# Kernel optimization log

Hardware: AMD Instinct MI355X
Metric: run time of the kernel (lower is better)

Reference implementation:

```python
import jax, jax.numpy as jnp
import numpy as np

IN_CH = 256
BOT = IN_CH // 2  # bottleneck channels
B, W, H = 4, 64, 64


def setup_inputs() -> dict:
    key = jax.random.key(0)
    ks = jax.random.split(key, 10)
    s_in = 1.0 / np.sqrt(IN_CH)   # torch Conv2d default init scale (kaiming-ish bound)
    s_bt = 1.0 / np.sqrt(BOT)
    return {
        "X": jax.random.normal(ks[0], (B, IN_CH, W, H), dtype=jnp.float32),
        "Wq": jax.random.uniform(ks[1], (BOT, IN_CH), jnp.float32, -s_in, s_in),
        "bq": jax.random.uniform(ks[2], (BOT,), jnp.float32, -s_in, s_in),
        "Wk": jax.random.uniform(ks[3], (BOT, IN_CH), jnp.float32, -s_in, s_in),
        "bk": jax.random.uniform(ks[4], (BOT,), jnp.float32, -s_in, s_in),
        "Wv": jax.random.uniform(ks[5], (BOT, IN_CH), jnp.float32, -s_in, s_in),
        "bv": jax.random.uniform(ks[6], (BOT,), jnp.float32, -s_in, s_in),
        "Wo": jax.random.uniform(ks[7], (IN_CH, BOT), jnp.float32, -s_bt, s_bt),
        "bo": jax.random.uniform(ks[8], (IN_CH,), jnp.float32, -s_bt, s_bt),
        "gamma": 0.1 * jax.random.normal(ks[9], (1,), dtype=jnp.float32),
    }


def reference(X, Wq, bq, Wk, bk, Wv, bv, Wo, bo, gamma):
    b, c, w, h = X.shape
    n = w * h
    Xf = X.reshape(b, c, n)  # [b, c, n] — 1x1 conv == per-pixel linear
    q = jnp.einsum('oc,bcn->bon', Wq, Xf) + bq[None, :, None]  # [b, c/2, n]
    k = jnp.einsum('oc,bcn->bon', Wk, Xf) + bk[None, :, None]
    v = jnp.einsum('oc,bcn->bon', Wv, Xf) + bv[None, :, None]
    # score[b,i,j] = sum_c q[b,c,i] * k[b,c,j]; softmax over dim=1 (query index i)
    score = jnp.einsum('bci,bcj->bij', q, k)          # [b, n, n]
    attn = jax.nn.softmax(score, axis=1)
    out = jnp.einsum('bci,bij->bcj', v, attn)         # [b, c/2, n]
    out = jnp.einsum('oc,bcn->bon', Wo, out) + bo[None, :, None]  # [b, c, n]
    out = out.reshape(b, c, w, h)
    return gamma[0] * out + X
```

## Files before the change

### kernel.cpp

```cpp
#include <hip/hip_runtime.h>
#include <math.h>

#define NBATCH 4
#define CIN    256
#define CBOT   128
#define NPIX   4096
#define NPART  4
#define LOG2E  1.44269504f

typedef __attribute__((ext_vector_type(4))) float f32x4;
typedef __attribute__((ext_vector_type(8))) short bf16x8;

__device__ __forceinline__ unsigned short f2bf(float f) {
    union { float f; unsigned u; } v; v.f = f;
    unsigned r = (v.u + 0x7FFFu + ((v.u >> 16) & 1u)) >> 16;
    return (unsigned short)r;
}

__global__ __launch_bounds__(256) void k_wcvt(
    const float* __restrict__ Wq, const float* __restrict__ Wk,
    const float* __restrict__ Wv, const float* __restrict__ Wo,
    unsigned short* __restrict__ Wb)
{
    const int f4 = (blockIdx.x * 256 + threadIdx.x) * 4;
    const int reg = f4 >> 15, loc = f4 & 32767;
    const float* __restrict__ W = (reg == 0) ? Wq : (reg == 1) ? Wk : (reg == 2) ? Wv : Wo;
    const float sc = (reg == 1) ? LOG2E : 1.f;
    float4 v = *(const float4*)(W + loc);
    ushort4 u;
    u.x = f2bf(v.x * sc); u.y = f2bf(v.y * sc);
    u.z = f2bf(v.z * sc); u.w = f2bf(v.w * sc);
    *(ushort4*)&Wb[f4] = u;
}

__global__ __launch_bounds__(256) void k_xt(
    const float* __restrict__ X, unsigned short* __restrict__ Xt)
{
    __shared__ float T[64][65];
    const int tid = threadIdx.x;
    const int pbase = blockIdx.x * 64;
    const int c0    = blockIdx.y * 64;
    const int b     = blockIdx.z;
#pragma unroll
    for (int k = 0; k < 4; ++k) {
        int f = tid + 256 * k;
        int cl = f >> 4, p4 = (f & 15) << 2;
        float4 v = *(const float4*)(X + (size_t)b * CIN * NPIX + (size_t)(c0 + cl) * NPIX + pbase + p4);
        T[cl][p4 + 0] = v.x; T[cl][p4 + 1] = v.y;
        T[cl][p4 + 2] = v.z; T[cl][p4 + 3] = v.w;
    }
    __syncthreads();
#pragma unroll
    for (int k = 0; k < 4; ++k) {
        int f = tid + 256 * k;
        int p = f >> 4, c4 = (f & 15) << 2;
        ushort4 u;
        u.x = f2bf(T[c4 + 0][p]); u.y = f2bf(T[c4 + 1][p]);
        u.z = f2bf(T[c4 + 2][p]); u.w = f2bf(T[c4 + 3][p]);
        *(ushort4*)&Xt[((size_t)b * NPIX + pbase + p) * CIN + c0 + c4] = u;
    }
}

__global__ __launch_bounds__(256) void k_qkv(
    const unsigned short* __restrict__ Xt,
    const unsigned short* __restrict__ Wb,
    const float* __restrict__ bq, const float* __restrict__ bk,
    const float* __restrict__ bv,
    unsigned short* __restrict__ Qt, unsigned short* __restrict__ Kt,
    unsigned short* __restrict__ Vt)
{
    const int tid = threadIdx.x;
    const int wv = tid >> 6, lane = tid & 63;
    const int grp = lane & 15, quad = lane >> 4;
    const int pbase = blockIdx.x * 32;
    const int b     = blockIdx.y;
    const unsigned short* __restrict__ Xb  = Xt + (size_t)b * NPIX * CIN;
    const unsigned short* __restrict__ Wqb = Wb;
    const unsigned short* __restrict__ Wkb = Wb + 32768;
    const unsigned short* __restrict__ Wvb = Wb + 65536;
    const int obase = 32 * wv;

    f32x4 aQ[2][2], aK[2][2], aV[2][2];
#pragma unroll
    for (int mt = 0; mt < 2; ++mt)
#pragma unroll
        for (int nt = 0; nt < 2; ++nt) {
            aQ[mt][nt] = (f32x4)0.f; aK[mt][nt] = (f32x4)0.f; aV[mt][nt] = (f32x4)0.f;
        }

    for (int ks = 0; ks < 8; ++ks) {
        bf16x8 bx[2];
#pragma unroll
        for (int nt = 0; nt < 2; ++nt)
            bx[nt] = *(const bf16x8*)&Xb[(size_t)(pbase + nt * 16 + grp) * CIN + ks * 32 + quad * 8];
        bf16x8 wq_[2], wk_[2], wv_[2];
#pragma unroll
        for (int mt = 0; mt < 2; ++mt) {
            const size_t roff = (size_t)(obase + mt * 16 + grp) * CIN + ks * 32 + quad * 8;
            wq_[mt] = *(const bf16x8*)&Wqb[roff];
            wk_[mt] = *(const bf16x8*)&Wkb[roff];
            wv_[mt] = *(const bf16x8*)&Wvb[roff];
        }
#pragma unroll
        for (int mt = 0; mt < 2; ++mt)
#pragma unroll
            for (int nt = 0; nt < 2; ++nt) {
                aQ[mt][nt] = __builtin_amdgcn_mfma_f32_16x16x32_bf16(wq_[mt], bx[nt], aQ[mt][nt], 0, 0, 0);
                aK[mt][nt] = __builtin_amdgcn_mfma_f32_16x16x32_bf16(wk_[mt], bx[nt], aK[mt][nt], 0, 0, 0);
                aV[mt][nt] = __builtin_amdgcn_mfma_f32_16x16x32_bf16(bx[mt], wv_[nt], aV[mt][nt], 0, 0, 0);
            }
    }

    unsigned short* Qb_ = Qt + (size_t)b * NPIX * CBOT;
    unsigned short* Kb_ = Kt + (size_t)b * NPIX * CBOT;
#pragma unroll
    for (int mt = 0; mt < 2; ++mt) {
        int o0 = obase + mt * 16 + quad * 4;
        float b4q[4], b4k[4];
#pragma unroll
        for (int r = 0; r < 4; ++r) { b4q[r] = bq[o0 + r]; b4k[r] = bk[o0 + r] * LOG2E; }
#pragma unroll
        for (int nt = 0; nt < 2; ++nt) {
            int p = pbase + nt * 16 + grp;
            ushort4 uq, uk;
            uq.x = f2bf(aQ[mt][nt][0] + b4q[0]); uq.y = f2bf(aQ[mt][nt][1] + b4q[1]);
            uq.z = f2bf(aQ[mt][nt][2] + b4q[2]); uq.w = f2bf(aQ[mt][nt][3] + b4q[3]);
            uk.x = f2bf(aK[mt][nt][0] + b4k[0]); uk.y = f2bf(aK[mt][nt][1] + b4k[1]);
            uk.z = f2bf(aK[mt][nt][2] + b4k[2]); uk.w = f2bf(aK[mt][nt][3] + b4k[3]);
            *(ushort4*)&Qb_[(size_t)p * CBOT + o0] = uq;
            *(ushort4*)&Kb_[(size_t)p * CBOT + o0] = uk;
        }
    }
    unsigned short* Vb_ = Vt + (size_t)b * CBOT * NPIX;
#pragma unroll
    for (int nt = 0; nt < 2; ++nt) {
        int o = obase + nt * 16 + grp;
        float bb = bv[o];
#pragma unroll
        for (int mt = 0; mt < 2; ++mt) {
            int p0 = pbase + mt * 16 + quad * 4;
            ushort4 u;
            u.x = f2bf(aV[mt][nt][0] + bb); u.y = f2bf(aV[mt][nt][1] + bb);
            u.z = f2bf(aV[mt][nt][2] + bb); u.w = f2bf(aV[mt][nt][3] + bb);
            *(ushort4*)&Vb_[(size_t)o * NPIX + p0] = u;
        }
    }
}

__global__ __launch_bounds__(256, 2) void k_flash(
    const unsigned short* __restrict__ Qt,
    const unsigned short* __restrict__ Kt,
    const unsigned short* __restrict__ Vt,
    unsigned short* __restrict__ Opart,
    float* __restrict__ Lpart)
{
    __shared__ __align__(16) unsigned short Qs[64][136];
    __shared__ __align__(16) unsigned short Vs[128][72];
    __shared__ __align__(16) unsigned short Ps[128][72];
    const int tid  = threadIdx.x;
    const int wv   = tid >> 6, lane = tid & 63;
    const int grp  = lane & 15, quad = lane >> 4;
    const int jblk = blockIdx.x * 128;
    const int part = blockIdx.y;
    const int b    = blockIdx.z;
    const int tbeg = part * (64 / NPART);
    const int tend = tbeg + (64 / NPART);
    const unsigned short* __restrict__ Qb = Qt + (size_t)b * NPIX * CBOT;
    const unsigned short* __restrict__ Kb = Kt + (size_t)b * NPIX * CBOT;
    const unsigned short* __restrict__ Vb = Vt + (size_t)b * CBOT * NPIX;

    bf16x8 aq[2][4];
#pragma unroll
    for (int set = 0; set < 2; ++set)
#pragma unroll
        for (int ks = 0; ks < 4; ++ks)
            aq[set][ks] = *(const bf16x8*)&Kb[
                (size_t)(jblk + wv * 32 + set * 16 + grp) * CBOT + ks * 32 + quad * 8];

    bf16x8 bones;
#pragma unroll
    for (int t = 0; t < 8; ++t) bones[t] = (short)0x3F80;

    f32x4 o[2][8];
#pragma unroll
    for (int set = 0; set < 2; ++set)
#pragma unroll
        for (int ct = 0; ct < 8; ++ct) o[set][ct] = (f32x4)0.f;
    f32x4 lacc[2] = {(f32x4)0.f, (f32x4)0.f};

    const int qrow = tid >> 4, qch = tid & 15;
    const int vrow = tid >> 3, vch = tid & 7;
    bf16x8 qreg[4], vreg[4];
#pragma unroll
    for (int k = 0; k < 4; ++k) {
        qreg[k] = *(const bf16x8*)&Qb[(size_t)(tbeg * 64 + qrow + 16 * k) * CBOT + qch * 8];
        vreg[k] = *(const bf16x8*)&Vb[(size_t)(vrow + 32 * k) * NPIX + tbeg * 64 + vch * 8];
    }

    for (int it = tbeg; it < tend; ++it) {
        __syncthreads();
#pragma unroll
        for (int k = 0; k < 4; ++k) {
            *(bf16x8*)&Qs[qrow + 16 * k][qch * 8] = qreg[k];
            *(bf16x8*)&Vs[vrow + 32 * k][vch * 8] = vreg[k];
        }
        __syncthreads();
        if (it + 1 < tend) {
            const int i1 = (it + 1) * 64;
#pragma unroll
            for (int k = 0; k < 4; ++k) {
                qreg[k] = *(const bf16x8*)&Qb[(size_t)(i1 + qrow + 16 * k) * CBOT + qch * 8];
                vreg[k] = *(const bf16x8*)&Vb[(size_t)(vrow + 32 * k) * NPIX + i1 + vch * 8];
            }
        }

        f32x4 sf[2][4];
#pragma unroll
        for (int set = 0; set < 2; ++set)
#pragma unroll
            for (int nt = 0; nt < 4; ++nt) sf[set][nt] = (f32x4)0.f;
#pragma unroll
        for (int nt = 0; nt < 4; ++nt)
#pragma unroll
            for (int ks = 0; ks < 4; ++ks) {
                bf16x8 bq_ = *(const bf16x8*)&Qs[nt * 16 + grp][ks * 32 + quad * 8];
                sf[0][nt] = __builtin_amdgcn_mfma_f32_16x16x32_bf16(aq[0][ks], bq_, sf[0][nt], 0, 0, 0);
                sf[1][nt] = __builtin_amdgcn_mfma_f32_16x16x32_bf16(aq[1][ks], bq_, sf[1][nt], 0, 0, 0);
            }

#pragma unroll
        for (int set = 0; set < 2; ++set)
#pragma unroll
            for (int nt = 0; nt < 4; ++nt)
#pragma unroll
                for (int r = 0; r < 4; ++r)
                    Ps[wv * 32 + set * 16 + quad * 4 + r][nt * 16 + grp] =
                        f2bf(exp2f(sf[set][nt][r]));

        bf16x8 af[2][2];
#pragma unroll
        for (int set = 0; set < 2; ++set)
#pragma unroll
            for (int ks2 = 0; ks2 < 2; ++ks2)
                af[set][ks2] = *(const bf16x8*)&Ps[wv * 32 + set * 16 + grp][ks2 * 32 + quad * 8];

#pragma unroll
        for (int ct = 0; ct < 8; ++ct)
#pragma unroll
            for (int ks2 = 0; ks2 < 2; ++ks2) {
                bf16x8 bv_ = *(const bf16x8*)&Vs[ct * 16 + grp][ks2 * 32 + quad * 8];
                o[0][ct] = __builtin_amdgcn_mfma_f32_16x16x32_bf16(af[0][ks2], bv_, o[0][ct], 0, 0, 0);
                o[1][ct] = __builtin_amdgcn_mfma_f32_16x16x32_bf16(af[1][ks2], bv_, o[1][ct], 0, 0, 0);
            }
#pragma unroll
        for (int set = 0; set < 2; ++set) {
            lacc[set] = __builtin_amdgcn_mfma_f32_16x16x32_bf16(af[set][0], bones, lacc[set], 0, 0, 0);
            lacc[set] = __builtin_amdgcn_mfma_f32_16x16x32_bf16(af[set][1], bones, lacc[set], 0, 0, 0);
        }
    }

    unsigned short* Ob = Opart + ((size_t)(part * NBATCH + b) * NPIX + jblk) * CBOT;
#pragma unroll
    for (int set = 0; set < 2; ++set)
#pragma unroll
        for (int ct = 0; ct < 8; ++ct)
#pragma unroll
            for (int r = 0; r < 4; ++r)
                Ob[(size_t)(wv * 32 + set * 16 + quad * 4 + r) * CBOT + ct * 16 + grp] =
                    f2bf(o[set][ct][r]);
    if (grp == 0) {
#pragma unroll
        for (int set = 0; set < 2; ++set)
#pragma unroll
            for (int r = 0; r < 4; ++r)
                Lpart[(size_t)(part * NBATCH + b) * NPIX + jblk + wv * 32 + set * 16 + quad * 4 + r] =
                    lacc[set][r];
    }
}

__global__ __launch_bounds__(256) void k_oproj(
    const unsigned short* __restrict__ Opart, const float* __restrict__ Lpart,
    const unsigned short* __restrict__ Wob, const float* __restrict__ bo,
    const float* __restrict__ gamma, const float* __restrict__ X,
    float* __restrict__ Out)
{
    const int tid = threadIdx.x;
    const int wv = tid >> 6, lane = tid & 63;
    const int grp = lane & 15, quad = lane >> 4;
    const int pbase = blockIdx.x * 32;
    const int b     = blockIdx.y;
    const int obase = 64 * wv;

    f32x4 acc[2][4];
#pragma unroll
    for (int mt = 0; mt < 2; ++mt)
#pragma unroll
        for (int nt = 0; nt < 4; ++nt) acc[mt][nt] = (f32x4)0.f;

    for (int ks = 0; ks < 4; ++ks) {
        bf16x8 bw[4];
#pragma unroll
        for (int nt = 0; nt < 4; ++nt)
            bw[nt] = *(const bf16x8*)&Wob[(size_t)(obase + nt * 16 + grp) * CBOT + ks * 32 + quad * 8];
#pragma unroll
        for (int mt = 0; mt < 2; ++mt) {
            int p = pbase + mt * 16 + grp;
#pragma unroll
            for (int part = 0; part < NPART; ++part) {
                bf16x8 ao = *(const bf16x8*)&Opart[
                    ((size_t)(part * NBATCH + b) * NPIX + p) * CBOT + ks * 32 + quad * 8];
#pragma unroll
                for (int nt = 0; nt < 4; ++nt)
                    acc[mt][nt] = __builtin_amdgcn_mfma_f32_16x16x32_bf16(ao, bw[nt], acc[mt][nt], 0, 0, 0);
            }
        }
    }

    float linv[2][4];
#pragma unroll
    for (int mt = 0; mt < 2; ++mt)
#pragma unroll
        for (int r = 0; r < 4; ++r) {
            int p = pbase + mt * 16 + quad * 4 + r;
            float ls = 0.f;
#pragma unroll
            for (int part = 0; part < NPART; ++part)
                ls += Lpart[(size_t)(part * NBATCH + b) * NPIX + p];
            linv[mt][r] = 1.f / ls;
        }
    float g = gamma[0];
#pragma unroll
    for (int nt = 0; nt < 4; ++nt) {
        int o = obase + nt * 16 + grp;
        float bb = bo[o];
#pragma unroll
        for (int mt = 0; mt < 2; ++mt) {
            int p0 = pbase + mt * 16 + quad * 4;
            size_t base = (size_t)b * CIN * NPIX + (size_t)o * NPIX + p0;
            float4 x4 = *(const float4*)(X + base);
            float4 r4;
            r4.x = g * (acc[mt][nt][0] * linv[mt][0] + bb) + x4.x;
            r4.y = g * (acc[mt][nt][1] * linv[mt][1] + bb) + x4.y;
            r4.z = g * (acc[mt][nt][2] * linv[mt][2] + bb) + x4.z;
            r4.w = g * (acc[mt][nt][3] * linv[mt][3] + bb) + x4.w;
            *(float4*)(Out + base) = r4;
        }
    }
}

extern "C" void kernel_launch(void* const* d_in, const int* in_sizes, int n_in,
                              void* d_out, int out_size, void* d_ws, size_t ws_size,
                              hipStream_t stream)
{
    (void)in_sizes; (void)n_in; (void)out_size; (void)ws_size;
    const float* X     = (const float*)d_in[0];
    const float* Wq    = (const float*)d_in[1];
    const float* bq    = (const float*)d_in[2];
    const float* Wk    = (const float*)d_in[3];
    const float* bk    = (const float*)d_in[4];
    const float* Wv    = (const float*)d_in[5];
    const float* bv    = (const float*)d_in[6];
    const float* Wo    = (const float*)d_in[7];
    const float* bo    = (const float*)d_in[8];
    const float* gamma = (const float*)d_in[9];
    float* out = (float*)d_out;

    const size_t BNC = (size_t)NBATCH * NPIX * CBOT;
    unsigned short* Qt    = (unsigned short*)d_ws;
    unsigned short* Kt    = Qt + BNC;
    unsigned short* Vt    = Kt + BNC;
    unsigned short* Opart = Vt + BNC;
    unsigned short* Xt    = Opart;
    float*          Lpart = (float*)(Opart + (size_t)NPART * BNC);
    unsigned short* Wb    = (unsigned short*)(Lpart + (size_t)NPART * NBATCH * NPIX);

    k_wcvt <<<dim3(128),               256, 0, stream>>>(Wq, Wk, Wv, Wo, Wb);
    k_xt   <<<dim3(64, 4, NBATCH),     256, 0, stream>>>(X, Xt);
    k_qkv  <<<dim3(128, NBATCH),       256, 0, stream>>>(Xt, Wb, bq, bk, bv, Qt, Kt, Vt);
    k_flash<<<dim3(32, NPART, NBATCH), 256, 0, stream>>>(Qt, Kt, Vt, Opart, Lpart);
    k_oproj<<<dim3(128, NBATCH),       256, 0, stream>>>(Opart, Lpart, Wb + 98304, bo, gamma, X, out);
}
```

Measured before the change: 174.5 us.

## Fuse QKV, flash, and output projection into persistent kernel with grid barriers

Merges weight conversion into the X transpose kernel. The QKV projection, flash attention and output projection kernels become one 512-block kernel separated by software grid barriers built on atomics. The aim is to remove launch overhead and inter-kernel gaps across five launches. It relies on all 512 blocks being co-resident (launch bounds of 2 blocks per CU, 256 CUs). The barrier has a spin timeout that could silently break correctness, and it adds atomic spin cost.

```diff
diff --git a/kernel.cpp b/kernel.cpp
--- a/kernel.cpp
+++ b/kernel.cpp
@@ -6,6 +6,7 @@
 #define CBOT   128
 #define NPIX   4096
 #define NPART  4
+#define NBLK   512
 #define LOG2E  1.44269504f
 
 typedef __attribute__((ext_vector_type(4))) float f32x4;
@@ -17,27 +18,52 @@
     return (unsigned short)r;
 }
 
-__global__ __launch_bounds__(256) void k_wcvt(
+__device__ __forceinline__ void gridbar(unsigned* cnt, unsigned* gen) {
+    __syncthreads();
+    if (threadIdx.x == 0) {
+        unsigned g = __hip_atomic_load(gen, __ATOMIC_RELAXED, __HIP_MEMORY_SCOPE_AGENT);
+        unsigned a = __hip_atomic_fetch_add(cnt, 1u, __ATOMIC_ACQ_REL, __HIP_MEMORY_SCOPE_AGENT);
+        if (a == NBLK - 1u) {
+            __hip_atomic_store(cnt, 0u, __ATOMIC_RELAXED, __HIP_MEMORY_SCOPE_AGENT);
+            __hip_atomic_store(gen, g + 1u, __ATOMIC_RELEASE, __HIP_MEMORY_SCOPE_AGENT);
+        } else {
+            int spins = 0;
+            while (__hip_atomic_load(gen, __ATOMIC_ACQUIRE, __HIP_MEMORY_SCOPE_AGENT) == g) {
+                __builtin_amdgcn_s_sleep(2);
+                if (++spins > (1 << 22)) break;
+            }
+        }
+    }
+    __syncthreads();
+}
+
+__global__ __launch_bounds__(256) void k_prep(
+    const float* __restrict__ X,
     const float* __restrict__ Wq, const float* __restrict__ Wk,
     const float* __restrict__ Wv, const float* __restrict__ Wo,
-    unsigned short* __restrict__ Wb)
-{
-    const int f4 = (blockIdx.x * 256 + threadIdx.x) * 4;
-    const int reg = f4 >> 15, loc = f4 & 32767;
-    const float* __restrict__ W = (reg == 0) ? Wq : (reg == 1) ? Wk : (reg == 2) ? Wv : Wo;
-    const float sc = (reg == 1) ? LOG2E : 1.f;
-    float4 v = *(const float4*)(W + loc);
-    ushort4 u;
-    u.x = f2bf(v.x * sc); u.y = f2bf(v.y * sc);
-    u.z = f2bf(v.z * sc); u.w = f2bf(v.w * sc);
-    *(ushort4*)&Wb[f4] = u;
-}
-
-__global__ __launch_bounds__(256) void k_xt(
-    const float* __restrict__ X, unsigned short* __restrict__ Xt)
+    unsigned short* __restrict__ Xt, unsigned short* __restrict__ Wb,
+    unsigned* __restrict__ Bar)
 {
     __shared__ float T[64][65];
     const int tid = threadIdx.x;
+    if (blockIdx.y == 4) {
+        const int gid = blockIdx.z * 64 + blockIdx.x;
+        if (gid < 128) {
+            const int f4 = (gid * 256 + tid) * 4;
+            const int reg = f4 >> 15, loc = f4 & 32767;
+            const float* __restrict__ W = (reg == 0) ? Wq : (reg == 1) ? Wk
+                                        : (reg == 2) ? Wv : Wo;
+            const float sc = (reg == 1) ? LOG2E : 1.f;
+            float4 v = *(const float4*)(W + loc);
+            ushort4 u;
+            u.x = f2bf(v.x * sc); u.y = f2bf(v.y * sc);
+            u.z = f2bf(v.z * sc); u.w = f2bf(v.w * sc);
+            *(ushort4*)&Wb[f4] = u;
+        } else if (gid == 128 && tid < 8) {
+            Bar[tid] = 0u;
+        }
+        return;
+    }
     const int pbase = blockIdx.x * 64;
     const int c0    = blockIdx.y * 64;
     const int b     = blockIdx.z;
@@ -61,289 +87,286 @@
     }
 }
 
-__global__ __launch_bounds__(256) void k_qkv(
-    const unsigned short* __restrict__ Xt,
+__global__ __launch_bounds__(256, 2) void k_mega(
+    const unsigned short* Xt,
     const unsigned short* __restrict__ Wb,
     const float* __restrict__ bq, const float* __restrict__ bk,
     const float* __restrict__ bv,
     unsigned short* __restrict__ Qt, unsigned short* __restrict__ Kt,
-    unsigned short* __restrict__ Vt)
-{
-    const int tid = threadIdx.x;
-    const int wv = tid >> 6, lane = tid & 63;
-    const int grp = lane & 15, quad = lane >> 4;
-    const int pbase = blockIdx.x * 32;
-    const int b     = blockIdx.y;
-    const unsigned short* __restrict__ Xb  = Xt + (size_t)b * NPIX * CIN;
-    const unsigned short* __restrict__ Wqb = Wb;
-    const unsigned short* __restrict__ Wkb = Wb + 32768;
-    const unsigned short* __restrict__ Wvb = Wb + 65536;
-    const int obase = 32 * wv;
-
-    f32x4 aQ[2][2], aK[2][2], aV[2][2];
-#pragma unroll
-    for (int mt = 0; mt < 2; ++mt)
-#pragma unroll
-        for (int nt = 0; nt < 2; ++nt) {
-            aQ[mt][nt] = (f32x4)0.f; aK[mt][nt] = (f32x4)0.f; aV[mt][nt] = (f32x4)0.f;
-        }
-
-    for (int ks = 0; ks < 8; ++ks) {
-        bf16x8 bx[2];
-#pragma unroll
-        for (int nt = 0; nt < 2; ++nt)
-            bx[nt] = *(const bf16x8*)&Xb[(size_t)(pbase + nt * 16 + grp) * CIN + ks * 32 + quad * 8];
-        bf16x8 wq_[2], wk_[2], wv_[2];
-#pragma unroll
-        for (int mt = 0; mt < 2; ++mt) {
-            const size_t roff = (size_t)(obase + mt * 16 + grp) * CIN + ks * 32 + quad * 8;
-            wq_[mt] = *(const bf16x8*)&Wqb[roff];
-            wk_[mt] = *(const bf16x8*)&Wkb[roff];
-            wv_[mt] = *(const bf16x8*)&Wvb[roff];
-        }
-#pragma unroll
-        for (int mt = 0; mt < 2; ++mt)
-#pragma unroll
-            for (int nt = 0; nt < 2; ++nt) {
-                aQ[mt][nt] = __builtin_amdgcn_mfma_f32_16x16x32_bf16(wq_[mt], bx[nt], aQ[mt][nt], 0, 0, 0);
-                aK[mt][nt] = __builtin_amdgcn_mfma_f32_16x16x32_bf16(wk_[mt], bx[nt], aK[mt][nt], 0, 0, 0);
-                aV[mt][nt] = __builtin_amdgcn_mfma_f32_16x16x32_bf16(bx[mt], wv_[nt], aV[mt][nt], 0, 0, 0);
-            }
-    }
-
-    unsigned short* Qb_ = Qt + (size_t)b * NPIX * CBOT;
-    unsigned short* Kb_ = Kt + (size_t)b * NPIX * CBOT;
-#pragma unroll
-    for (int mt = 0; mt < 2; ++mt) {
-        int o0 = obase + mt * 16 + quad * 4;
-        float b4q[4], b4k[4];
-#pragma unroll
-        for (int r = 0; r < 4; ++r) { b4q[r] = bq[o0 + r]; b4k[r] = bk[o0 + r] * LOG2E; }
-#pragma unroll
-        for (int nt = 0; nt < 2; ++nt) {
-            int p = pbase + nt * 16 + grp;
-            ushort4 uq, uk;
-            uq.x = f2bf(aQ[mt][nt][0] + b4q[0]); uq.y = f2bf(aQ[mt][nt][1] + b4q[1]);
-            uq.z = f2bf(aQ[mt][nt][2] + b4q[2]); uq.w = f2bf(aQ[mt][nt][3] + b4q[3]);
-            uk.x = f2bf(aK[mt][nt][0] + b4k[0]); uk.y = f2bf(aK[mt][nt][1] + b4k[1]);
-            uk.z = f2bf(aK[mt][nt][2] + b4k[2]); uk.w = f2bf(aK[mt][nt][3] + b4k[3]);
-            *(ushort4*)&Qb_[(size_t)p * CBOT + o0] = uq;
-            *(ushort4*)&Kb_[(size_t)p * CBOT + o0] = uk;
-        }
-    }
-    unsigned short* Vb_ = Vt + (size_t)b * CBOT * NPIX;
-#pragma unroll
-    for (int nt = 0; nt < 2; ++nt) {
-        int o = obase + nt * 16 + grp;
-        float bb = bv[o];
-#pragma unroll
-        for (int mt = 0; mt < 2; ++mt) {
-            int p0 = pbase + mt * 16 + quad * 4;
-            ushort4 u;
-            u.x = f2bf(aV[mt][nt][0] + bb); u.y = f2bf(aV[mt][nt][1] + bb);
-            u.z = f2bf(aV[mt][nt][2] + bb); u.w = f2bf(aV[mt][nt][3] + bb);
-            *(ushort4*)&Vb_[(size_t)o * NPIX + p0] = u;
-        }
-    }
-}
-
-__global__ __launch_bounds__(256, 2) void k_flash(
-    const unsigned short* __restrict__ Qt,
-    const unsigned short* __restrict__ Kt,
-    const unsigned short* __restrict__ Vt,
-    unsigned short* __restrict__ Opart,
-    float* __restrict__ Lpart)
+    unsigned short* __restrict__ Vt,
+    unsigned short* Opart, float* __restrict__ Lpart,
+    const float* __restrict__ bo, const float* __restrict__ gamma,
+    const float* __restrict__ X, float* __restrict__ Out,
+    unsigned* Bar)
 {
     __shared__ __align__(16) unsigned short Qs[64][136];
     __shared__ __align__(16) unsigned short Vs[128][72];
     __shared__ __align__(16) unsigned short Ps[128][72];
+
     const int tid  = threadIdx.x;
+    const int bid  = blockIdx.x;
     const int wv   = tid >> 6, lane = tid & 63;
     const int grp  = lane & 15, quad = lane >> 4;
-    const int jblk = blockIdx.x * 128;
-    const int part = blockIdx.y;
-    const int b    = blockIdx.z;
-    const int tbeg = part * (64 / NPART);
-    const int tend = tbeg + (64 / NPART);
-    const unsigned short* __restrict__ Qb = Qt + (size_t)b * NPIX * CBOT;
-    const unsigned short* __restrict__ Kb = Kt + (size_t)b * NPIX * CBOT;
-    const unsigned short* __restrict__ Vb = Vt + (size_t)b * CBOT * NPIX;
-
-    bf16x8 aq[2][4];
-#pragma unroll
-    for (int set = 0; set < 2; ++set)
-#pragma unroll
-        for (int ks = 0; ks < 4; ++ks)
-            aq[set][ks] = *(const bf16x8*)&Kb[
-                (size_t)(jblk + wv * 32 + set * 16 + grp) * CBOT + ks * 32 + quad * 8];
-
-    bf16x8 bones;
-#pragma unroll
-    for (int t = 0; t < 8; ++t) bones[t] = (short)0x3F80;
-
-    f32x4 o[2][8];
-#pragma unroll
-    for (int set = 0; set < 2; ++set)
-#pragma unroll
-        for (int ct = 0; ct < 8; ++ct) o[set][ct] = (f32x4)0.f;
-    f32x4 lacc[2] = {(f32x4)0.f, (f32x4)0.f};
-
-    const int qrow = tid >> 4, qch = tid & 15;
-    const int vrow = tid >> 3, vch = tid & 7;
-    bf16x8 qreg[4], vreg[4];
-#pragma unroll
-    for (int k = 0; k < 4; ++k) {
-        qreg[k] = *(const bf16x8*)&Qb[(size_t)(tbeg * 64 + qrow + 16 * k) * CBOT + qch * 8];
-        vreg[k] = *(const bf16x8*)&Vb[(size_t)(vrow + 32 * k) * NPIX + tbeg * 64 + vch * 8];
-    }
-
-    for (int it = tbeg; it < tend; ++it) {
-        __syncthreads();
+
+    {
+        const int pbase = (bid & 127) * 32;
+        const int b     = bid >> 7;
+        const unsigned short* Xb  = Xt + (size_t)b * NPIX * CIN;
+        const unsigned short* __restrict__ Wqb = Wb;
+        const unsigned short* __restrict__ Wkb = Wb + 32768;
+        const unsigned short* __restrict__ Wvb = Wb + 65536;
+        const int obase = 32 * wv;
+
+        f32x4 aQ[2][2], aK[2][2], aV[2][2];
+#pragma unroll
+        for (int mt = 0; mt < 2; ++mt)
+#pragma unroll
+            for (int nt = 0; nt < 2; ++nt) {
+                aQ[mt][nt] = (f32x4)0.f; aK[mt][nt] = (f32x4)0.f; aV[mt][nt] = (f32x4)0.f;
+            }
+
+        for (int ks = 0; ks < 8; ++ks) {
+            bf16x8 bx[2];
+#pragma unroll
+            for (int nt = 0; nt < 2; ++nt)
+                bx[nt] = *(const bf16x8*)&Xb[(size_t)(pbase + nt * 16 + grp) * CIN + ks * 32 + quad * 8];
+            bf16x8 wq_[2], wk_[2], wv_[2];
+#pragma unroll
+            for (int mt = 0; mt < 2; ++mt) {
+                const size_t roff = (size_t)(obase + mt * 16 + grp) * CIN + ks * 32 + quad * 8;
+                wq_[mt] = *(const bf16x8*)&Wqb[roff];
+                wk_[mt] = *(const bf16x8*)&Wkb[roff];
+                wv_[mt] = *(const bf16x8*)&Wvb[roff];
+            }
+#pragma unroll
+            for (int mt = 0; mt < 2; ++mt)
+#pragma unroll
+                for (int nt = 0; nt < 2; ++nt) {
+                    aQ[mt][nt] = __builtin_amdgcn_mfma_f32_16x16x32_bf16(wq_[mt], bx[nt], aQ[mt][nt], 0, 0, 0);
+                    aK[mt][nt] = __builtin_amdgcn_mfma_f32_16x16x32_bf16(wk_[mt], bx[nt], aK[mt][nt], 0, 0, 0);
+                    aV[mt][nt] = __builtin_amdgcn_mfma_f32_16x16x32_bf16(bx[mt], wv_[nt], aV[mt][nt], 0, 0, 0);
+                }
+        }
+
+        unsigned short* Qb_ = Qt + (size_t)b * NPIX * CBOT;
+        unsigned short* Kb_ = Kt + (size_t)b * NPIX * CBOT;
+#pragma unroll
+        for (int mt = 0; mt < 2; ++mt) {
+            int o0 = obase + mt * 16 + quad * 4;
+            float b4q[4], b4k[4];
+#pragma unroll
+            for (int r = 0; r < 4; ++r) { b4q[r] = bq[o0 + r]; b4k[r] = bk[o0 + r] * LOG2E; }
+#pragma unroll
+            for (int nt = 0; nt < 2; ++nt) {
+                int p = pbase + nt * 16 + grp;
+                ushort4 uq, uk;
+                uq.x = f2bf(aQ[mt][nt][0] + b4q[0]); uq.y = f2bf(aQ[mt][nt][1] + b4q[1]);
+                uq.z = f2bf(aQ[mt][nt][2] + b4q[2]); uq.w = f2bf(aQ[mt][nt][3] + b4q[3]);
+                uk.x = f2bf(aK[mt][nt][0] + b4k[0]); uk.y = f2bf(aK[mt][nt][1] + b4k[1]);
+                uk.z = f2bf(aK[mt][nt][2] + b4k[2]); uk.w = f2bf(aK[mt][nt][3] + b4k[3]);
+                *(ushort4*)&Qb_[(size_t)p * CBOT + o0] = uq;
+                *(ushort4*)&Kb_[(size_t)p * CBOT + o0] = uk;
+            }
+        }
+        unsigned short* Vb_ = Vt + (size_t)b * CBOT * NPIX;
+#pragma unroll
+        for (int nt = 0; nt < 2; ++nt) {
+            int o = obase + nt * 16 + grp;
+            float bb = bv[o];
+#pragma unroll
+            for (int mt = 0; mt < 2; ++mt) {
+                int p0 = pbase + mt * 16 + quad * 4;
+                ushort4 u;
+                u.x = f2bf(aV[mt][nt][0] + bb); u.y = f2bf(aV[mt][nt][1] + bb);
+                u.z = f2bf(aV[mt][nt][2] + bb); u.w = f2bf(aV[mt][nt][3] + bb);
+                *(ushort4*)&Vb_[(size_t)o * NPIX + p0] = u;
+            }
+        }
+    }
+
+    gridbar(Bar, Bar + 1);
+
+    {
+        const int jblk = (bid & 31) * 128;
+        const int part = (bid >> 5) & 3;
+        const int b    = bid >> 7;
+        const int tbeg = part * (64 / NPART);
+        const int tend = tbeg + (64 / NPART);
+        const unsigned short* __restrict__ Qb = Qt + (size_t)b * NPIX * CBOT;
+        const unsigned short* __restrict__ Kb = Kt + (size_t)b * NPIX * CBOT;
+        const unsigned short* __restrict__ Vb = Vt + (size_t)b * CBOT * NPIX;
+
+        bf16x8 aq[2][4];
+#pragma unroll
+        for (int set = 0; set < 2; ++set)
+#pragma unroll
+            for (int ks = 0; ks < 4; ++ks)
+                aq[set][ks] = *(const bf16x8*)&Kb[
+                    (size_t)(jblk + wv * 32 + set * 16 + grp) * CBOT + ks * 32 + quad * 8];
+
+        bf16x8 bones;
+#pragma unroll
+        for (int t = 0; t < 8; ++t) bones[t] = (short)0x3F80;
+
+        f32x4 o[2][8];
+#pragma unroll
+        for (int set = 0; set < 2; ++set)
+#pragma unroll
+            for (int ct = 0; ct < 8; ++ct) o[set][ct] = (f32x4)0.f;
+        f32x4 lacc[2] = {(f32x4)0.f, (f32x4)0.f};
+
+        const int qrow = tid >> 4, qch = tid & 15;
+        const int vrow = tid >> 3, vch = tid & 7;
+        bf16x8 qreg[4], vreg[4];
 #pragma unroll
         for (int k = 0; k < 4; ++k) {
-            *(bf16x8*)&Qs[qrow + 16 * k][qch * 8] = qreg[k];
-            *(bf16x8*)&Vs[vrow + 32 * k][vch * 8] = vreg[k];
-        }
-        __syncthreads();
-        if (it + 1 < tend) {
-            const int i1 = (it + 1) * 64;
+            qreg[k] = *(const bf16x8*)&Qb[(size_t)(tbeg * 64 + qrow + 16 * k) * CBOT + qch * 8];
+            vreg[k] = *(const bf16x8*)&Vb[(size_t)(vrow + 32 * k) * NPIX + tbeg * 64 + vch * 8];
+        }
+
+        for (int it = tbeg; it < tend; ++it) {
+            __syncthreads();
 #pragma unroll
             for (int k = 0; k < 4; ++k) {
-                qreg[k] = *(const bf16x8*)&Qb[(size_t)(i1 + qrow + 16 * k) * CBOT + qch * 8];
-                vreg[k] = *(const bf16x8*)&Vb[(size_t)(vrow + 32 * k) * NPIX + i1 + vch * 8];
-            }
-        }
-
-        f32x4 sf[2][4];
+                *(bf16x8*)&Qs[qrow + 16 * k][qch * 8] = qreg[k];
+                *(bf16x8*)&Vs[vrow + 32 * k][vch * 8] = vreg[k];
+            }
+            __syncthreads();
+            if (it + 1 < tend) {
+                const int i1 = (it + 1) * 64;
+#pragma unroll
+                for (int k = 0; k < 4; ++k) {
+                    qreg[k] = *(const bf16x8*)&Qb[(size_t)(i1 + qrow + 16 * k) * CBOT + qch * 8];
+                    vreg[k] = *(const bf16x8*)&Vb[(size_t)(vrow + 32 * k) * NPIX + i1 + vch * 8];
+                }
+            }
+
+            f32x4 sf[2][4];
+#pragma unroll
+            for (int set = 0; set < 2; ++set)
+#pragma unroll
+                for (int nt = 0; nt < 4; ++nt) sf[set][nt] = (f32x4)0.f;
+#pragma unroll
+            for (int nt = 0; nt < 4; ++nt)
+#pragma unroll
+                for (int ks = 0; ks < 4; ++ks) {
+                    bf16x8 bq_ = *(const bf16x8*)&Qs[nt * 16 + grp][ks * 32 + quad * 8];
+                    sf[0][nt] = __builtin_amdgcn_mfma_f32_16x16x32_bf16(aq[0][ks], bq_, sf[0][nt], 0, 0, 0);
+                    sf[1][nt] = __builtin_amdgcn_mfma_f32_16x16x32_bf16(aq[1][ks], bq_, sf[1][nt], 0, 0, 0);
+                }
+
+#pragma unroll
+            for (int set = 0; set < 2; ++set)
+#pragma unroll
+                for (int nt = 0; nt < 4; ++nt)
+#pragma unroll
+                    for (int r = 0; r < 4; ++r)
+                        Ps[wv * 32 + set * 16 + quad * 4 + r][nt * 16 + grp] =
+                            f2bf(exp2f(sf[set][nt][r]));
+
+            bf16x8 af[2][2];
+#pragma unroll
+            for (int set = 0; set < 2; ++set)
+#pragma unroll
+                for (int ks2 = 0; ks2 < 2; ++ks2)
+                    af[set][ks2] = *(const bf16x8*)&Ps[wv * 32 + set * 16 + grp][ks2 * 32 + quad * 8];
+
+#pragma unroll
+            for (int ct = 0; ct < 8; ++ct)
+#pragma unroll
+                for (int ks2 = 0; ks2 < 2; ++ks2) {
+                    bf16x8 bv_ = *(const bf16x8*)&Vs[ct * 16 + grp][ks2 * 32 + quad * 8];
+                    o[0][ct] = __builtin_amdgcn_mfma_f32_16x16x32_bf16(af[0][ks2], bv_, o[0][ct], 0, 0, 0);
+                    o[1][ct] = __builtin_amdgcn_mfma_f32_16x16x32_bf16(af[1][ks2], bv_, o[1][ct], 0, 0, 0);
+                }
+#pragma unroll
+            for (int set = 0; set < 2; ++set) {
+                lacc[set] = __builtin_amdgcn_mfma_f32_16x16x32_bf16(af[set][0], bones, lacc[set], 0, 0, 0);
+                lacc[set] = __builtin_amdgcn_mfma_f32_16x16x32_bf16(af[set][1], bones, lacc[set], 0, 0, 0);
+            }
+        }
+
+        unsigned short* Ob = Opart + ((size_t)(part * NBATCH + b) * NPIX + jblk) * CBOT;
 #pragma unroll
         for (int set = 0; set < 2; ++set)
 #pragma unroll
-            for (int nt = 0; nt < 4; ++nt) sf[set][nt] = (f32x4)0.f;
-#pragma unroll
-        for (int nt = 0; nt < 4; ++nt)
-#pragma unroll
-            for (int ks = 0; ks < 4; ++ks) {
-                bf16x8 bq_ = *(const bf16x8*)&Qs[nt * 16 + grp][ks * 32 + quad * 8];
-                sf[0][nt] = __builtin_amdgcn_mfma_f32_16x16x32_bf16(aq[0][ks], bq_, sf[0][nt], 0, 0, 0);
-                sf[1][nt] = __builtin_amdgcn_mfma_f32_16x16x32_bf16(aq[1][ks], bq_, sf[1][nt], 0, 0, 0);
-            }
-
-#pragma unroll
-        for (int set = 0; set < 2; ++set)
+            for (int ct = 0; ct < 8; ++ct)
+#pragma unroll
+                for (int r = 0; r < 4; ++r)
+                    Ob[(size_t)(wv * 32 + set * 16 + quad * 4 + r) * CBOT + ct * 16 + grp] =
+                        f2bf(o[set][ct][r]);
+        if (grp == 0) {
+#pragma unroll
+            for (int set = 0; set < 2; ++set)
+#pragma unroll
+                for (int r = 0; r < 4; ++r)
+                    Lpart[(size_t)(part * NBATCH + b) * NPIX + jblk + wv * 32 + set * 16 + quad * 4 + r] =
+                        lacc[set][r];
+        }
+    }
+
+    gridbar(Bar, Bar + 1);
+
+    {
+        const int pbase = (bid & 127) * 32;
+        const int b     = bid >> 7;
+        const unsigned short* __restrict__ Wob = Wb + 98304;
+        const int obase = 64 * wv;
+
+        f32x4 acc[2][4];
+#pragma unroll
+        for (int mt = 0; mt < 2; ++mt)
+#pragma unroll
+            for (int nt = 0; nt < 4; ++nt) acc[mt][nt] = (f32x4)0.f;
+
+        for (int ks = 0; ks < 4; ++ks) {
+            bf16x8 bw[4];
 #pragma unroll
             for (int nt = 0; nt < 4; ++nt)
-#pragma unroll
-                for (int r = 0; r < 4; ++r)
-                    Ps[wv * 32 + set * 16 + quad * 4 + r][nt * 16 + grp] =
-                        f2bf(exp2f(sf[set][nt][r]));
-
-        bf16x8 af[2][2];
-#pragma unroll
-        for (int set = 0; set < 2; ++set)
-#pragma unroll
-            for (int ks2 = 0; ks2 < 2; ++ks2)
-                af[set][ks2] = *(const bf16x8*)&Ps[wv * 32 + set * 16 + grp][ks2 * 32 + quad * 8];
-
-#pragma unroll
-        for (int ct = 0; ct < 8; ++ct)
-#pragma unroll
-            for (int ks2 = 0; ks2 < 2; ++ks2) {
-                bf16x8 bv_ = *(const bf16x8*)&Vs[ct * 16 + grp][ks2 * 32 + quad * 8];
-                o[0][ct] = __builtin_amdgcn_mfma_f32_16x16x32_bf16(af[0][ks2], bv_, o[0][ct], 0, 0, 0);
-                o[1][ct] = __builtin_amdgcn_mfma_f32_16x16x32_bf16(af[1][ks2], bv_, o[1][ct], 0, 0, 0);
-            }
-#pragma unroll
-        for (int set = 0; set < 2; ++set) {
-            lacc[set] = __builtin_amdgcn_mfma_f32_16x16x32_bf16(af[set][0], bones, lacc[set], 0, 0, 0);
-            lacc[set] = __builtin_amdgcn_mfma_f32_16x16x32_bf16(af[set][1], bones, lacc[set], 0, 0, 0);
-        }
-    }
-
-    unsigned short* Ob = Opart + ((size_t)(part * NBATCH + b) * NPIX + jblk) * CBOT;
-#pragma unroll
-    for (int set = 0; set < 2; ++set)
-#pragma unroll
-        for (int ct = 0; ct < 8; ++ct)
-#pragma unroll
-            for (int r = 0; r < 4; ++r)
-                Ob[(size_t)(wv * 32 + set * 16 + quad * 4 + r) * CBOT + ct * 16 + grp] =
-                    f2bf(o[set][ct][r]);
-    if (grp == 0) {
-#pragma unroll
-        for (int set = 0; set < 2; ++set)
-#pragma unroll
-            for (int r = 0; r < 4; ++r)
-                Lpart[(size_t)(part * NBATCH + b) * NPIX + jblk + wv * 32 + set * 16 + quad * 4 + r] =
-                    lacc[set][r];
-    }
-}
-
-__global__ __launch_bounds__(256) void k_oproj(
-    const unsigned short* __restrict__ Opart, const float* __restrict__ Lpart,
-    const unsigned short* __restrict__ Wob, const float* __restrict__ bo,
-    const float* __restrict__ gamma, const float* __restrict__ X,
-    float* __restrict__ Out)
-{
-    const int tid = threadIdx.x;
-    const int wv = tid >> 6, lane = tid & 63;
-    const int grp = lane & 15, quad = lane >> 4;
-    const int pbase = blockIdx.x * 32;
-    const int b     = blockIdx.y;
-    const int obase = 64 * wv;
-
-    f32x4 acc[2][4];
-#pragma unroll
-    for (int mt = 0; mt < 2; ++mt)
-#pragma unroll
-        for (int nt = 0; nt < 4; ++nt) acc[mt][nt] = (f32x4)0.f;
-
-    for (int ks = 0; ks < 4; ++ks) {
-        bf16x8 bw[4];
-#pragma unroll
-        for (int nt = 0; nt < 4; ++nt)
-            bw[nt] = *(const bf16x8*)&Wob[(size_t)(obase + nt * 16 + grp) * CBOT + ks * 32 + quad * 8];
-#pragma unroll
-        for (int mt = 0; mt < 2; ++mt) {
-            int p = pbase + mt * 16 + grp;
-#pragma unroll
-            for (int part = 0; part < NPART; ++part) {
-                bf16x8 ao = *(const bf16x8*)&Opart[
-                    ((size_t)(part * NBATCH + b) * NPIX + p) * CBOT + ks * 32 + quad * 8];
-#pragma unroll
-                for (int nt = 0; nt < 4; ++nt)
-                    acc[mt][nt] = __builtin_amdgcn_mfma_f32_16x16x32_bf16(ao, bw[nt], acc[mt][nt], 0, 0, 0);
-            }
-        }
-    }
-
-    float linv[2][4];
-#pragma unroll
-    for (int mt = 0; mt < 2; ++mt)
-#pragma unroll
-        for (int r = 0; r < 4; ++r) {
-            int p = pbase + mt * 16 + quad * 4 + r;
-            float ls = 0.f;
-#pragma unroll
-            for (int part = 0; part < NPART; ++part)
-                ls += Lpart[(size_t)(part * NBATCH + b) * NPIX + p];
-            linv[mt][r] = 1.f / ls;
-        }
-    float g = gamma[0];
-#pragma unroll
-    for (int nt = 0; nt < 4; ++nt) {
-        int o = obase + nt * 16 + grp;
-        float bb = bo[o];
-#pragma unroll
-        for (int mt = 0; mt < 2; ++mt) {
-            int p0 = pbase + mt * 16 + quad * 4;
-            size_t base = (size_t)b * CIN * NPIX + (size_t)o * NPIX + p0;
-            float4 x4 = *(const float4*)(X + base);
-            float4 r4;
-            r4.x = g * (acc[mt][nt][0] * linv[mt][0] + bb) + x4.x;
-            r4.y = g * (acc[mt][nt][1] * linv[mt][1] + bb) + x4.y;
-            r4.z = g * (acc[mt][nt][2] * linv[mt][2] + bb) + x4.z;
-            r4.w = g * (acc[mt][nt][3] * linv[mt][3] + bb) + x4.w;
-            *(float4*)(Out + base) = r4;
+                bw[nt] = *(const bf16x8*)&Wob[(size_t)(obase + nt * 16 + grp) * CBOT + ks * 32 + quad * 8];
+#pragma unroll
+            for (int mt = 0; mt < 2; ++mt) {
+                int p = pbase + mt * 16 + grp;
+#pragma unroll
+                for (int part = 0; part < NPART; ++part) {
+                    bf16x8 ao = *(const bf16x8*)&Opart[
+                        ((size_t)(part * NBATCH + b) * NPIX + p) * CBOT + ks * 32 + quad * 8];
+#pragma unroll
+                    for (int nt = 0; nt < 4; ++nt)
+                        acc[mt][nt] = __builtin_amdgcn_mfma_f32_16x16x32_bf16(ao, bw[nt], acc[mt][nt], 0, 0, 0);
+                }
+            }
+        }
+
+        float linv[2][4];
+#pragma unroll
+        for (int mt = 0; mt < 2; ++mt)
+#pragma unroll
+            for (int r = 0; r < 4; ++r) {
+                int p = pbase + mt * 16 + quad * 4 + r;
+                float ls = 0.f;
+#pragma unroll
+                for (int part = 0; part < NPART; ++part)
+                    ls += Lpart[(size_t)(part * NBATCH + b) * NPIX + p];
+                linv[mt][r] = 1.f / ls;
+            }
+        float g = gamma[0];
+#pragma unroll
+        for (int nt = 0; nt < 4; ++nt) {
+            int o = obase + nt * 16 + grp;
+            float bb = bo[o];
+#pragma unroll
+            for (int mt = 0; mt < 2; ++mt) {
+                int p0 = pbase + mt * 16 + quad * 4;
+                size_t base = (size_t)b * CIN * NPIX + (size_t)o * NPIX + p0;
+                float4 x4 = *(const float4*)(X + base);
+                float4 r4;
+                r4.x = g * (acc[mt][nt][0] * linv[mt][0] + bb) + x4.x;
+                r4.y = g * (acc[mt][nt][1] * linv[mt][1] + bb) + x4.y;
+                r4.z = g * (acc[mt][nt][2] * linv[mt][2] + bb) + x4.z;
+                r4.w = g * (acc[mt][nt][3] * linv[mt][3] + bb) + x4.w;
+                *(float4*)(Out + base) = r4;
+            }
         }
     }
 }
@@ -373,10 +396,9 @@
     unsigned short* Xt    = Opart;
     float*          Lpart = (float*)(Opart + (size_t)NPART * BNC);
     unsigned short* Wb    = (unsigned short*)(Lpart + (size_t)NPART * NBATCH * NPIX);
-
-    k_wcvt <<<dim3(128),               256, 0, stream>>>(Wq, Wk, Wv, Wo, Wb);
-    k_xt   <<<dim3(64, 4, NBATCH),     256, 0, stream>>>(X, Xt);
-    k_qkv  <<<dim3(128, NBATCH),       256, 0, stream>>>(Xt, Wb, bq, bk, bv, Qt, Kt, Vt);
-    k_flash<<<dim3(32, NPART, NBATCH), 256, 0, stream>>>(Qt, Kt, Vt, Opart, Lpart);
-    k_oproj<<<dim3(128, NBATCH),       256, 0, stream>>>(Opart, Lpart, Wb + 98304, bo, gamma, X, out);
+    unsigned*       Bar   = (unsigned*)(Wb + 131072);
+
+    k_prep<<<dim3(64, 5, NBATCH), 256, 0, stream>>>(X, Wq, Wk, Wv, Wo, Xt, Wb, Bar);
+    k_mega<<<dim3(NBLK), 256, 0, stream>>>(Xt, Wb, bq, bk, bv, Qt, Kt, Vt,
+                                           Opart, Lpart, bo, gamma, X, out, Bar);
 }
```

After: 324.5 us. 1.86x slower.

## Fuse X transpose into QKV projection and use packed bf16 conversion and fast exp2

Applied to the files above, without the earlier changes.

Removes the separate k_xt transpose kernel: the QKV projection now loads fp32 X directly, converts it to bf16 and transposes it into shared memory before the MFMA loop. This drops one launch and the global round trip of the transposed X buffer. Scalar bf16 rounding is replaced by the hardware packed cvt_pk_bf16_f32 builtin where available, and exp2f in the flash softmax uses the raw amdgcn exp2 intrinsic. The packed conversion may round differently from the manual rounding, and the raw exp2 skips denormal handling.

```diff
diff --git a/kernel.cpp b/kernel.cpp
--- a/kernel.cpp
+++ b/kernel.cpp
@@ -16,6 +16,21 @@
     unsigned r = (v.u + 0x7FFFu + ((v.u >> 16) & 1u)) >> 16;
     return (unsigned short)r;
 }
+__device__ __forceinline__ unsigned pk2bf(float a, float b) {
+#if __has_builtin(__builtin_amdgcn_cvt_pk_bf16_f32)
+    auto r = __builtin_amdgcn_cvt_pk_bf16_f32(a, b);
+    unsigned u; __builtin_memcpy(&u, &r, 4); return u;
+#else
+    return (unsigned)f2bf(a) | ((unsigned)f2bf(b) << 16);
+#endif
+}
+__device__ __forceinline__ float fexp2(float x) {
+#if __has_builtin(__builtin_amdgcn_exp2f)
+    return __builtin_amdgcn_exp2f(x);
+#else
+    return exp2f(x);
+#endif
+}
 
 __global__ __launch_bounds__(256) void k_wcvt(
     const float* __restrict__ Wq, const float* __restrict__ Wk,
@@ -27,54 +42,40 @@
     const float* __restrict__ W = (reg == 0) ? Wq : (reg == 1) ? Wk : (reg == 2) ? Wv : Wo;
     const float sc = (reg == 1) ? LOG2E : 1.f;
     float4 v = *(const float4*)(W + loc);
-    ushort4 u;
-    u.x = f2bf(v.x * sc); u.y = f2bf(v.y * sc);
-    u.z = f2bf(v.z * sc); u.w = f2bf(v.w * sc);
-    *(ushort4*)&Wb[f4] = u;
-}
-
-__global__ __launch_bounds__(256) void k_xt(
-    const float* __restrict__ X, unsigned short* __restrict__ Xt)
-{
-    __shared__ float T[64][65];
-    const int tid = threadIdx.x;
-    const int pbase = blockIdx.x * 64;
-    const int c0    = blockIdx.y * 64;
-    const int b     = blockIdx.z;
-#pragma unroll
-    for (int k = 0; k < 4; ++k) {
-        int f = tid + 256 * k;
-        int cl = f >> 4, p4 = (f & 15) << 2;
-        float4 v = *(const float4*)(X + (size_t)b * CIN * NPIX + (size_t)(c0 + cl) * NPIX + pbase + p4);
-        T[cl][p4 + 0] = v.x; T[cl][p4 + 1] = v.y;
-        T[cl][p4 + 2] = v.z; T[cl][p4 + 3] = v.w;
-    }
-    __syncthreads();
-#pragma unroll
-    for (int k = 0; k < 4; ++k) {
-        int f = tid + 256 * k;
-        int p = f >> 4, c4 = (f & 15) << 2;
-        ushort4 u;
-        u.x = f2bf(T[c4 + 0][p]); u.y = f2bf(T[c4 + 1][p]);
-        u.z = f2bf(T[c4 + 2][p]); u.w = f2bf(T[c4 + 3][p]);
-        *(ushort4*)&Xt[((size_t)b * NPIX + pbase + p) * CIN + c0 + c4] = u;
-    }
-}
-
-__global__ __launch_bounds__(256) void k_qkv(
-    const unsigned short* __restrict__ Xt,
+    uint2 u;
+    u.x = pk2bf(v.x * sc, v.y * sc);
+    u.y = pk2bf(v.z * sc, v.w * sc);
+    *(uint2*)&Wb[f4] = u;
+}
+
+__global__ __launch_bounds__(256) void k_qkvx(
+    const float* __restrict__ X,
     const unsigned short* __restrict__ Wb,
     const float* __restrict__ bq, const float* __restrict__ bk,
     const float* __restrict__ bv,
     unsigned short* __restrict__ Qt, unsigned short* __restrict__ Kt,
     unsigned short* __restrict__ Vt)
 {
+    __shared__ __align__(16) unsigned short Xs[32][264];
     const int tid = threadIdx.x;
     const int wv = tid >> 6, lane = tid & 63;
     const int grp = lane & 15, quad = lane >> 4;
     const int pbase = blockIdx.x * 32;
     const int b     = blockIdx.y;
-    const unsigned short* __restrict__ Xb  = Xt + (size_t)b * NPIX * CIN;
+    const float* __restrict__ Xg = X + (size_t)b * CIN * NPIX + pbase;
+
+#pragma unroll
+    for (int k = 0; k < 8; ++k) {
+        int f = tid + 256 * k;
+        int c = f >> 3, pg = (f & 7) << 2;
+        float4 v = *(const float4*)(Xg + (size_t)c * NPIX + pg);
+        Xs[pg + 0][c] = f2bf(v.x);
+        Xs[pg + 1][c] = f2bf(v.y);
+        Xs[pg + 2][c] = f2bf(v.z);
+        Xs[pg + 3][c] = f2bf(v.w);
+    }
+    __syncthreads();
+
     const unsigned short* __restrict__ Wqb = Wb;
     const unsigned short* __restrict__ Wkb = Wb + 32768;
     const unsigned short* __restrict__ Wvb = Wb + 65536;
@@ -92,7 +93,7 @@
         bf16x8 bx[2];
 #pragma unroll
         for (int nt = 0; nt < 2; ++nt)
-            bx[nt] = *(const bf16x8*)&Xb[(size_t)(pbase + nt * 16 + grp) * CIN + ks * 32 + quad * 8];
+            bx[nt] = *(const bf16x8*)&Xs[nt * 16 + grp][ks * 32 + quad * 8];
         bf16x8 wq_[2], wk_[2], wv_[2];
 #pragma unroll
         for (int mt = 0; mt < 2; ++mt) {
@@ -122,13 +123,13 @@
 #pragma unroll
         for (int nt = 0; nt < 2; ++nt) {
             int p = pbase + nt * 16 + grp;
-            ushort4 uq, uk;
-            uq.x = f2bf(aQ[mt][nt][0] + b4q[0]); uq.y = f2bf(aQ[mt][nt][1] + b4q[1]);
-            uq.z = f2bf(aQ[mt][nt][2] + b4q[2]); uq.w = f2bf(aQ[mt][nt][3] + b4q[3]);
-            uk.x = f2bf(aK[mt][nt][0] + b4k[0]); uk.y = f2bf(aK[mt][nt][1] + b4k[1]);
-            uk.z = f2bf(aK[mt][nt][2] + b4k[2]); uk.w = f2bf(aK[mt][nt][3] + b4k[3]);
-            *(ushort4*)&Qb_[(size_t)p * CBOT + o0] = uq;
-            *(ushort4*)&Kb_[(size_t)p * CBOT + o0] = uk;
+            uint2 uq, uk;
+            uq.x = pk2bf(aQ[mt][nt][0] + b4q[0], aQ[mt][nt][1] + b4q[1]);
+            uq.y = pk2bf(aQ[mt][nt][2] + b4q[2], aQ[mt][nt][3] + b4q[3]);
+            uk.x = pk2bf(aK[mt][nt][0] + b4k[0], aK[mt][nt][1] + b4k[1]);
+            uk.y = pk2bf(aK[mt][nt][2] + b4k[2], aK[mt][nt][3] + b4k[3]);
+            *(uint2*)&Qb_[(size_t)p * CBOT + o0] = uq;
+            *(uint2*)&Kb_[(size_t)p * CBOT + o0] = uk;
         }
     }
     unsigned short* Vb_ = Vt + (size_t)b * CBOT * NPIX;
@@ -139,10 +140,10 @@
 #pragma unroll
         for (int mt = 0; mt < 2; ++mt) {
             int p0 = pbase + mt * 16 + quad * 4;
-            ushort4 u;
-            u.x = f2bf(aV[mt][nt][0] + bb); u.y = f2bf(aV[mt][nt][1] + bb);
-            u.z = f2bf(aV[mt][nt][2] + bb); u.w = f2bf(aV[mt][nt][3] + bb);
-            *(ushort4*)&Vb_[(size_t)o * NPIX + p0] = u;
+            uint2 u;
+            u.x = pk2bf(aV[mt][nt][0] + bb, aV[mt][nt][1] + bb);
+            u.y = pk2bf(aV[mt][nt][2] + bb, aV[mt][nt][3] + bb);
+            *(uint2*)&Vb_[(size_t)o * NPIX + p0] = u;
         }
     }
 }
@@ -229,13 +230,19 @@
             }
 
 #pragma unroll
-        for (int set = 0; set < 2; ++set)
-#pragma unroll
-            for (int nt = 0; nt < 4; ++nt)
-#pragma unroll
-                for (int r = 0; r < 4; ++r)
-                    Ps[wv * 32 + set * 16 + quad * 4 + r][nt * 16 + grp] =
-                        f2bf(exp2f(sf[set][nt][r]));
+        for (int set = 0; set < 2; ++set) {
+            const int rbase = wv * 32 + set * 16 + quad * 4;
+#pragma unroll
+            for (int nt = 0; nt < 4; ++nt) {
+                const int col = nt * 16 + grp;
+                unsigned u01 = pk2bf(fexp2(sf[set][nt][0]), fexp2(sf[set][nt][1]));
+                unsigned u23 = pk2bf(fexp2(sf[set][nt][2]), fexp2(sf[set][nt][3]));
+                Ps[rbase + 0][col] = (unsigned short)u01;
+                Ps[rbase + 1][col] = (unsigned short)(u01 >> 16);
+                Ps[rbase + 2][col] = (unsigned short)u23;
+                Ps[rbase + 3][col] = (unsigned short)(u23 >> 16);
+            }
+        }
 
         bf16x8 af[2][2];
 #pragma unroll
@@ -370,13 +377,11 @@
     unsigned short* Kt    = Qt + BNC;
     unsigned short* Vt    = Kt + BNC;
     unsigned short* Opart = Vt + BNC;
-    unsigned short* Xt    = Opart;
     float*          Lpart = (float*)(Opart + (size_t)NPART * BNC);
     unsigned short* Wb    = (unsigned short*)(Lpart + (size_t)NPART * NBATCH * NPIX);
 
     k_wcvt <<<dim3(128),               256, 0, stream>>>(Wq, Wk, Wv, Wo, Wb);
-    k_xt   <<<dim3(64, 4, NBATCH),     256, 0, stream>>>(X, Xt);
-    k_qkv  <<<dim3(128, NBATCH),       256, 0, stream>>>(Xt, Wb, bq, bk, bv, Qt, Kt, Vt);
+    k_qkvx <<<dim3(128, NBATCH),       256, 0, stream>>>(X, Wb, bq, bk, bv, Qt, Kt, Vt);
     k_flash<<<dim3(32, NPART, NBATCH), 256, 0, stream>>>(Qt, Kt, Vt, Opart, Lpart);
     k_oproj<<<dim3(128, NBATCH),       256, 0, stream>>>(Opart, Lpart, Wb + 98304, bo, gamma, X, out);
 }
```

After: 160.8 us. 7.8% less time.
